# Kernel tuning notes

Measured on AMD Instinct MI355X. Metric: run time of the kernel, lower is better.

The kernel has to match this reference:

```python
import jax, jax.numpy as jnp
import numpy as np

N = 50000   # nodes
E = 800000  # edges
IN, H1, H2, OUT = 256, 512, 1024, 3000
EPS = 1e-5


def _glorot(key, fan_in, fan_out):
    s = jnp.sqrt(6.0 / (fan_in + fan_out)).astype(jnp.float32)
    return jax.random.uniform(key, (fan_in, fan_out), jnp.float32, -s, s)


def setup_inputs() -> dict:
    key = jax.random.key(0)
    ks = jax.random.split(key, 8)
    x = jax.random.normal(ks[0], (N, IN), jnp.float32)
    edge_index = jax.random.randint(ks[1], (2, E), 0, N, jnp.int64)
    edge_attr = jax.random.uniform(ks[2], (E, 3), jnp.float32)
    y = jnp.zeros((N,), jnp.int64)  # single domain -> plain BatchNorm path
    return {
        "x": x, "edge_index": edge_index, "edge_attr": edge_attr, "y": y,
        "W1": _glorot(ks[3], IN, H1), "b1": jnp.zeros((H1,), jnp.float32),
        "g1": jnp.ones((H1,), jnp.float32), "be1": jnp.zeros((H1,), jnp.float32),
        "W2": _glorot(ks[4], H1, H2), "b2": jnp.zeros((H2,), jnp.float32),
        "g2": jnp.ones((H2,), jnp.float32), "be2": jnp.zeros((H2,), jnp.float32),
        "W3": _glorot(ks[5], H2, OUT), "b3": jnp.zeros((OUT,), jnp.float32),
    }


def _gcn_layer(h_in, W, b, src, dst, w):
    # PyG GCNConv: x' = D^{-1/2}(A_w + I)D^{-1/2} x W + b, self-loop weight 1
    h = h_in @ W                                             # [N, F]
    deg = jax.ops.segment_sum(w, dst, num_segments=N) + 1.0  # weighted in-degree + self loop
    dinv = jax.lax.rsqrt(deg)                                # [N]
    coef = dinv[src] * w * dinv[dst]                         # [E]
    agg = jax.ops.segment_sum(coef[:, None] * h[src], dst, num_segments=N)
    return agg + (dinv * dinv)[:, None] * h + b              # self-loop term + bias


def _bn_relu(h, g, b):
    # BatchNorm1d in training mode (batch statistics, biased variance) + ReLU
    m = h.mean(axis=0)
    v = jnp.mean((h - m) ** 2, axis=0)
    return jax.nn.relu((h - m) * jax.lax.rsqrt(v + EPS) * g + b)


def reference(x, edge_index, edge_attr, y, W1, b1, g1, be1, W2, b2, g2, be2, W3, b3):
    src, dst = edge_index[0], edge_index[1]
    w = edge_attr[:, 2]
    h = _bn_relu(_gcn_layer(x, W1, b1, src, dst, w), g1, be1)
    h = _bn_relu(_gcn_layer(h, W2, b2, src, dst, w), g2, be2)
    return _gcn_layer(h, W3, b3, src, dst, w)
```

## Files before the change

kernel.cpp:

```cpp
#include <hip/hip_runtime.h>

#define NN 50000
#define NE 800000
#define EPSV 1e-5f

typedef _Float16 f16;
typedef __attribute__((ext_vector_type(4)))  float f32x4;
typedef __attribute__((ext_vector_type(16))) float f32x16;
typedef __attribute__((ext_vector_type(8)))  f16 f16x8;
typedef __attribute__((ext_vector_type(4)))  f16 f16x4;

static __device__ __forceinline__ int kperm(int k){
  int q = (k>>2)&3;
  int p = ((q&1)<<1) | (q>>1);
  return (k & ~15) + (p<<2) + (k&3);
}

__global__ void k_init_deg(float* __restrict__ deg){
  int i = blockIdx.x*256 + threadIdx.x;
  if (i < NN) deg[i] = 1.0f;
}

__global__ void k_build(const int* __restrict__ ei, const float* __restrict__ ea,
                        int* __restrict__ cnt, float* __restrict__ deg){
  int e = blockIdx.x*256 + threadIdx.x;
  if (e < NE){
    int d = ei[NE + e];
    atomicAdd(&cnt[d], 1);
    atomicAdd(&deg[d], ea[3*e+2]);
  }
}

__global__ void k_fin_deg(const float* __restrict__ deg, float* __restrict__ dinv,
                          float* __restrict__ dinv2){
  int i = blockIdx.x*256 + threadIdx.x;
  if (i < NN){ float r = rsqrtf(deg[i]); dinv[i] = r; dinv2[i] = r*r; }
}

__global__ __launch_bounds__(1024) void k_scan(const int* __restrict__ cnt,
                                               int* __restrict__ rowptr,
                                               int* __restrict__ cursor){
  __shared__ int sums[1024];
  int t = threadIdx.x;
  int b0 = t*49, b1 = b0+49; if (b0 > NN) b0 = NN; if (b1 > NN) b1 = NN;
  int s = 0;
  for (int i = b0; i < b1; ++i) s += cnt[i];
  sums[t] = s; __syncthreads();
  for (int o = 1; o < 1024; o <<= 1){
    int v = (t >= o) ? sums[t-o] : 0;
    __syncthreads();
    sums[t] += v;
    __syncthreads();
  }
  int p = sums[t] - s;
  for (int i = b0; i < b1; ++i){ rowptr[i] = p; cursor[i] = p; p += cnt[i]; }
  if (t == 1023) rowptr[NN] = sums[1023];
}

__global__ void k_fill(const int* __restrict__ ei, const float* __restrict__ ea,
                       const float* __restrict__ dinv, int* __restrict__ cursor,
                       int* __restrict__ csrc, float* __restrict__ ccf){
  int e = blockIdx.x*256 + threadIdx.x;
  if (e < NE){
    int s = ei[e], d = ei[NE+e];
    float w = ea[3*e+2];
    int p = atomicAdd(&cursor[d], 1);
    csrc[p] = s;
    ccf[p] = dinv[s]*w*dinv[d];
  }
}

__global__ void k_xconv(const float* __restrict__ x, f16* __restrict__ xh){
  int idx = blockIdx.x*256 + threadIdx.x;
  if (idx >= NN*64) return;
  int node = idx >> 6, k = (idx & 63)*4;
  f32x4 v = *(const f32x4*)(x + (size_t)node*256 + k);
  f16x4 h;
  #pragma unroll
  for (int j=0;j<4;++j) h[j] = (f16)v[j];
  *(f16x4*)(xh + (size_t)node*256 + kperm(k)) = h;
}

__global__ void k_w16(const float* __restrict__ W, f16* __restrict__ Wt,
                      int K, int M, int Mpad){
  int idx = blockIdx.x*256 + threadIdx.x;
  if (idx >= K*Mpad) return;
  int k = idx / Mpad, n = idx % Mpad;
  float v = (n < M) ? W[(size_t)k*M + n] : 0.f;
  Wt[(size_t)n*K + kperm(k)] = (f16)v;
}

template<int K, bool BN>
__global__ __launch_bounds__(256) void k_agg16(
    const f16* __restrict__ H, const int* __restrict__ rp,
    const int* __restrict__ cs, const float* __restrict__ cf,
    const float* __restrict__ dinv2,
    const float* __restrict__ s1, const float* __restrict__ s2,
    const float* __restrict__ g, const float* __restrict__ be,
    f16* __restrict__ outp)
{
  const int tid = threadIdx.x;
  int node, c;
  if (K == 256){
    node = blockIdx.x*8 + (tid>>5);
    c = (tid&31)*8;
  } else {
    node = blockIdx.x*4 + (tid>>6);
    c = (blockIdx.y<<9) + (tid&63)*8;
  }
  if (node >= NN) return;
  float av[8], bv[8];
  if (BN){
    int qa0 = kperm(c), qa1 = kperm(c+4);
    #pragma unroll
    for (int j=0;j<8;++j){
      int ac = (j<4) ? qa0+j : qa1+(j-4);
      float mm = s1[c+j]*(1.f/NN);
      float var = s2[c+j]*(1.f/NN) - mm*mm;
      float sc = rsqrtf(var+EPSV)*g[ac];
      av[j] = sc;
      bv[j] = fmaf(-mm, sc, be[ac]);
    }
  }
  f16x8 hv = *(const f16x8*)(H + (size_t)node*K + c);
  float d2 = dinv2[node];
  float acc[8];
  #pragma unroll
  for (int j=0;j<8;++j){
    float v = (float)hv[j];
    if (BN){ v = fmaf(v, av[j], bv[j]); v = v > 0.f ? v : 0.f; }
    acc[j] = d2*v;
  }
  int e0 = rp[node], e1 = rp[node+1];
  for (int e = e0; e < e1; ++e){
    int s = cs[e]; float w = cf[e];
    f16x8 v8 = *(const f16x8*)(H + (size_t)s*K + c);
    #pragma unroll
    for (int j=0;j<8;++j){
      float v = (float)v8[j];
      if (BN){ v = fmaf(v, av[j], bv[j]); v = v > 0.f ? v : 0.f; }
      acc[j] += w*v;
    }
  }
  f16x8 o;
  #pragma unroll
  for (int j=0;j<8;++j) o[j] = (f16)acc[j];
  *(f16x8*)(outp + (size_t)node*K + c) = o;
}

template<bool STATS>
__global__ __launch_bounds__(256) void k_gemm16(
    const f16* __restrict__ A, const f16* __restrict__ B,
    const float* __restrict__ bias, float* __restrict__ Cf,
    f16* __restrict__ Ch, float* __restrict__ s1, float* __restrict__ s2,
    int K, int M)
{
  __shared__ f16 Ah[2][4096];
  __shared__ f16 Bh[2][4096];
  const int tid  = threadIdx.x;
  const int lane = tid & 63;
  const int wave = tid >> 6;
  const int wr = wave >> 1, wc = wave & 1;

  int nwg = gridDim.x*gridDim.y;
  int bid = blockIdx.y*gridDim.x + blockIdx.x;
  if ((nwg & 7) == 0){
    int cpx = nwg >> 3;
    bid = (bid & 7)*cpx + (bid >> 3);
  }
  const int bx = bid % gridDim.x, by = bid / gridDim.x;
  const int row0 = by*128, col0 = bx*128;

  f32x16 acc[2][2];
  #pragma unroll
  for (int m=0;m<2;++m)
    #pragma unroll
    for (int n=0;n<2;++n)
      #pragma unroll
      for (int t=0;t<16;++t) acc[m][n][t] = 0.f;

  auto stage = [&](int buf, int k0){
    #pragma unroll
    for (int i=0;i<2;++i){
      int phys = i*256 + tid;
      int rr = phys >> 2, cp = phys & 3;
      int sc2 = cp ^ ((rr>>1)&3);
      const f16* srcA = A + (size_t)(row0+rr)*K + k0 + sc2*8;
      const f16* srcB = B + (size_t)(col0+rr)*K + k0 + sc2*8;
      f16* dstA = &Ah[buf][(size_t)(i*256 + (wave<<6))*8];
      f16* dstB = &Bh[buf][(size_t)(i*256 + (wave<<6))*8];
      __builtin_amdgcn_global_load_lds((const unsigned int*)srcA, (unsigned int*)dstA, 16, 0, 0);
      __builtin_amdgcn_global_load_lds((const unsigned int*)srcB, (unsigned int*)dstB, 16, 0, 0);
    }
  };

  stage(0, 0);
  __syncthreads();
  const int nT = K >> 5;
  for (int t = 0; t < nT; ++t){
    const int cur = t & 1;
    if (t + 1 < nT) stage(cur^1, (t+1) << 5);

    const int hg = lane >> 5;
    #pragma unroll
    for (int c2=0;c2<2;++c2){
      f16x8 fa[2], fb[2];
      #pragma unroll
      for (int m=0;m<2;++m){
        int r = wr*64 + m*32 + (lane&31);
        int u = c2*2 + hg;
        fa[m] = *(const f16x8*)&Ah[cur][r*32 + ((u ^ ((r>>1)&3))<<3)];
      }
      #pragma unroll
      for (int n=0;n<2;++n){
        int r = wc*64 + n*32 + (lane&31);
        int u = c2*2 + hg;
        fb[n] = *(const f16x8*)&Bh[cur][r*32 + ((u ^ ((r>>1)&3))<<3)];
      }
      #pragma unroll
      for (int m=0;m<2;++m)
        #pragma unroll
        for (int n=0;n<2;++n)
          acc[m][n] = __builtin_amdgcn_mfma_f32_32x32x16_f16(fa[m], fb[n], acc[m][n], 0,0,0);
    }
    __syncthreads();
  }

  #pragma unroll
  for (int n=0;n<2;++n){
    int cg = col0 + wc*64 + n*32 + (lane&31);
    if (STATS){
      int cp = kperm(cg);
      float sum = 0.f, sq = 0.f;
      #pragma unroll
      for (int m=0;m<2;++m){
        #pragma unroll
        for (int t=0;t<16;++t){
          int rg = row0 + wr*64 + m*32 + (t&3) + ((t>>2)&3)*8 + ((lane>>5)<<2);
          if (rg < NN){
            float v = acc[m][n][t];
            sum += v; sq += v*v;
            Ch[(size_t)rg*M + cp] = (f16)v;
          }
        }
      }
      atomicAdd(&s1[cp], sum);
      atomicAdd(&s2[cp], sq);
    } else {
      float bv = (cg < M) ? bias[cg] : 0.f;
      #pragma unroll
      for (int m=0;m<2;++m){
        #pragma unroll
        for (int t=0;t<16;++t){
          int rg = row0 + wr*64 + m*32 + (t&3) + ((t>>2)&3)*8 + ((lane>>5)<<2);
          if (rg < NN && cg < M)
            __builtin_nontemporal_store(acc[m][n][t] + bv, &Cf[(size_t)rg*M + cg]);
        }
      }
    }
  }
}

extern "C" void kernel_launch(void* const* d_in, const int* in_sizes, int n_in,
                              void* d_out, int out_size, void* d_ws, size_t ws_size,
                              hipStream_t stream){
  const float* x   = (const float*)d_in[0];
  const int*   ei  = (const int*)d_in[1];
  const float* ea  = (const float*)d_in[2];
  const float* W1  = (const float*)d_in[4];
  const float* g1  = (const float*)d_in[6];
  const float* be1 = (const float*)d_in[7];
  const float* W2  = (const float*)d_in[8];
  const float* g2  = (const float*)d_in[10];
  const float* be2 = (const float*)d_in[11];
  const float* W3  = (const float*)d_in[12];
  const float* b3  = (const float*)d_in[13];
  float* out = (float*)d_out;

  char* p = (char*)d_ws;
  int*   cnt    = (int*)p;   p += (size_t)NN*4;
  int*   cursor = (int*)p;   p += (size_t)NN*4;
  int*   rowptr = (int*)p;   p += (size_t)(NN+4)*4;
  float* deg    = (float*)p; p += (size_t)NN*4;
  float* dinv   = (float*)p; p += (size_t)NN*4;
  float* dinv2  = (float*)p; p += (size_t)NN*4;
  int*   csrc   = (int*)p;   p += (size_t)NE*4;
  float* ccf    = (float*)p; p += (size_t)NE*4;
  f16*   Wt     = (f16*)p;   p += (size_t)3072*1024*2;
  float* s1a    = (float*)p; p += 1024*4;
  float* s2a    = (float*)p; p += 1024*4;
  float* s1b    = (float*)p; p += 1024*4;
  float* s2b    = (float*)p; p += 1024*4;
  f16*   aggh   = (f16*)p;   p += (size_t)50176*1024*2;

  f16* xh  = (f16*)out;
  f16* h1h = xh  + (size_t)NN*256;
  f16* h2h = h1h + (size_t)NN*512;

  const int T = 256;
  const int gN = (NN+T-1)/T, gE = NE/T;
  const int GR = (NN+127)/128;

  hipMemsetAsync(cnt, 0, (size_t)NN*4, stream);
  hipMemsetAsync(s1a, 0, 4*1024*4, stream);
  k_init_deg<<<gN,T,0,stream>>>(deg);
  k_build<<<gE,T,0,stream>>>(ei, ea, cnt, deg);
  k_fin_deg<<<gN,T,0,stream>>>(deg, dinv, dinv2);
  k_scan<<<1,1024,0,stream>>>(cnt, rowptr, cursor);
  k_fill<<<gE,T,0,stream>>>(ei, ea, dinv, cursor, csrc, ccf);
  k_xconv<<<(NN*64+T-1)/T,T,0,stream>>>(x, xh);

  k_agg16<256,false><<<dim3(NN/8,1),T,0,stream>>>(xh, rowptr, csrc, ccf, dinv2,
                                                  nullptr,nullptr,nullptr,nullptr, aggh);
  k_w16<<<(256*512)/T,T,0,stream>>>(W1, Wt, 256, 512, 512);
  k_gemm16<true><<<dim3(4,GR),T,0,stream>>>(aggh, Wt, nullptr, nullptr, h1h, s1a, s2a, 256, 512);

  k_agg16<512,true><<<dim3(NN/4,1),T,0,stream>>>(h1h, rowptr, csrc, ccf, dinv2,
                                                 s1a, s2a, g1, be1, aggh);
  k_w16<<<(512*1024)/T,T,0,stream>>>(W2, Wt, 512, 1024, 1024);
  k_gemm16<true><<<dim3(8,GR),T,0,stream>>>(aggh, Wt, nullptr, nullptr, h2h, s1b, s2b, 512, 1024);

  k_agg16<1024,true><<<dim3(NN/4,2),T,0,stream>>>(h2h, rowptr, csrc, ccf, dinv2,
                                                  s1b, s2b, g2, be2, aggh);
  k_w16<<<(1024*3072)/T,T,0,stream>>>(W3, Wt, 1024, 3000, 3072);
  k_gemm16<false><<<dim3(24,GR),T,0,stream>>>(aggh, Wt, b3, out, nullptr, nullptr, nullptr, 1024, 3000);
}
```

Baseline: 1.700 ms.

## Enlarge GEMM tiles to 256x256 with K-step 64 and a new LDS swizzle

Replaces the 128x128 GEMM tile with a 256x256 output tile per 256-thread block, using a 4x4 array of 32x32 MFMA accumulators per wave and a K step of 64. Each thread now stages whole 128-byte row chunks through global_load_lds with an XOR-based swizzle on the column chunk. The goal is to double operand reuse per LDS byte and cut global/L2 traffic and the number of blocks for the three dense GEMMs. In exchange it uses 128 KB of LDS and far more accumulator registers, so only one block fits per CU. It also pads rows to 50176, which relies on the aggregation buffer's padding and on the Wt buffer having a 3072-column layout.

```diff
diff --git a/kernel.cpp b/kernel.cpp
--- a/kernel.cpp
+++ b/kernel.cpp
@@ -149,18 +149,20 @@
 }
 
 template<bool STATS>
-__global__ __launch_bounds__(256) void k_gemm16(
+__global__ __launch_bounds__(256,1) void k_gemm256(
     const f16* __restrict__ A, const f16* __restrict__ B,
     const float* __restrict__ bias, float* __restrict__ Cf,
     f16* __restrict__ Ch, float* __restrict__ s1, float* __restrict__ s2,
     int K, int M)
 {
-  __shared__ f16 Ah[2][4096];
-  __shared__ f16 Bh[2][4096];
+  __shared__ f16 Ah[2][16384];
+  __shared__ f16 Bh[2][16384];
   const int tid  = threadIdx.x;
   const int lane = tid & 63;
   const int wave = tid >> 6;
   const int wr = wave >> 1, wc = wave & 1;
+  const int hg = lane >> 5;
+  const int rl = lane & 31;
 
   int nwg = gridDim.x*gridDim.y;
   int bid = blockIdx.y*gridDim.x + blockIdx.x;
@@ -169,74 +171,74 @@
     bid = (bid & 7)*cpx + (bid >> 3);
   }
   const int bx = bid % gridDim.x, by = bid / gridDim.x;
-  const int row0 = by*128, col0 = bx*128;
-
-  f32x16 acc[2][2];
-  #pragma unroll
-  for (int m=0;m<2;++m)
-    #pragma unroll
-    for (int n=0;n<2;++n)
+  const int row0 = by*256, col0 = bx*256;
+
+  f32x16 acc[4][4];
+  #pragma unroll
+  for (int m=0;m<4;++m)
+    #pragma unroll
+    for (int n=0;n<4;++n)
       #pragma unroll
       for (int t=0;t<16;++t) acc[m][n][t] = 0.f;
 
+  const f16* rowA = A + (size_t)(row0 + tid)*K;
+  const f16* rowB = B + (size_t)(col0 + tid)*K;
+  const int xo = tid & 7;
+
   auto stage = [&](int buf, int k0){
     #pragma unroll
-    for (int i=0;i<2;++i){
-      int phys = i*256 + tid;
-      int rr = phys >> 2, cp = phys & 3;
-      int sc2 = cp ^ ((rr>>1)&3);
-      const f16* srcA = A + (size_t)(row0+rr)*K + k0 + sc2*8;
-      const f16* srcB = B + (size_t)(col0+rr)*K + k0 + sc2*8;
-      f16* dstA = &Ah[buf][(size_t)(i*256 + (wave<<6))*8];
-      f16* dstB = &Bh[buf][(size_t)(i*256 + (wave<<6))*8];
-      __builtin_amdgcn_global_load_lds((const unsigned int*)srcA, (unsigned int*)dstA, 16, 0, 0);
-      __builtin_amdgcn_global_load_lds((const unsigned int*)srcB, (unsigned int*)dstB, 16, 0, 0);
+    for (int i=0;i<8;++i){
+      int cA = i ^ xo;
+      f16* dstA = &Ah[buf][i*2048 + wave*512];
+      __builtin_amdgcn_global_load_lds((const unsigned int*)(rowA + k0 + cA*8),
+                                       (unsigned int*)dstA, 16, 0, 0);
+      f16* dstB = &Bh[buf][i*2048 + wave*512];
+      __builtin_amdgcn_global_load_lds((const unsigned int*)(rowB + k0 + cA*8),
+                                       (unsigned int*)dstB, 16, 0, 0);
     }
   };
 
   stage(0, 0);
   __syncthreads();
-  const int nT = K >> 5;
+  const int nT = K >> 6;
   for (int t = 0; t < nT; ++t){
     const int cur = t & 1;
-    if (t + 1 < nT) stage(cur^1, (t+1) << 5);
-
-    const int hg = lane >> 5;
-    #pragma unroll
-    for (int c2=0;c2<2;++c2){
-      f16x8 fa[2], fb[2];
-      #pragma unroll
-      for (int m=0;m<2;++m){
-        int r = wr*64 + m*32 + (lane&31);
-        int u = c2*2 + hg;
-        fa[m] = *(const f16x8*)&Ah[cur][r*32 + ((u ^ ((r>>1)&3))<<3)];
+    if (t + 1 < nT) stage(cur^1, (t+1) << 6);
+
+    #pragma unroll
+    for (int g=0; g<4; ++g){
+      const int u = g*2 + hg;
+      f16x8 fa[4], fb[4];
+      #pragma unroll
+      for (int m=0;m<4;++m){
+        int r = wr*128 + m*32 + rl;
+        fa[m] = *(const f16x8*)&Ah[cur][((u ^ (r&7))<<11) + (r<<3)];
       }
       #pragma unroll
-      for (int n=0;n<2;++n){
-        int r = wc*64 + n*32 + (lane&31);
-        int u = c2*2 + hg;
-        fb[n] = *(const f16x8*)&Bh[cur][r*32 + ((u ^ ((r>>1)&3))<<3)];
+      for (int n=0;n<4;++n){
+        int r = wc*128 + n*32 + rl;
+        fb[n] = *(const f16x8*)&Bh[cur][((u ^ (r&7))<<11) + (r<<3)];
       }
       #pragma unroll
-      for (int m=0;m<2;++m)
+      for (int m=0;m<4;++m)
         #pragma unroll
-        for (int n=0;n<2;++n)
+        for (int n=0;n<4;++n)
           acc[m][n] = __builtin_amdgcn_mfma_f32_32x32x16_f16(fa[m], fb[n], acc[m][n], 0,0,0);
     }
     __syncthreads();
   }
 
   #pragma unroll
-  for (int n=0;n<2;++n){
-    int cg = col0 + wc*64 + n*32 + (lane&31);
+  for (int n=0;n<4;++n){
+    int cg = col0 + wc*128 + n*32 + rl;
     if (STATS){
       int cp = kperm(cg);
       float sum = 0.f, sq = 0.f;
       #pragma unroll
-      for (int m=0;m<2;++m){
+      for (int m=0;m<4;++m){
         #pragma unroll
         for (int t=0;t<16;++t){
-          int rg = row0 + wr*64 + m*32 + (t&3) + ((t>>2)&3)*8 + ((lane>>5)<<2);
+          int rg = row0 + wr*128 + m*32 + (t&3) + ((t>>2)&3)*8 + (hg<<2);
           if (rg < NN){
             float v = acc[m][n][t];
             sum += v; sq += v*v;
@@ -249,10 +251,10 @@
     } else {
       float bv = (cg < M) ? bias[cg] : 0.f;
       #pragma unroll
-      for (int m=0;m<2;++m){
+      for (int m=0;m<4;++m){
         #pragma unroll
         for (int t=0;t<16;++t){
-          int rg = row0 + wr*64 + m*32 + (t&3) + ((t>>2)&3)*8 + ((lane>>5)<<2);
+          int rg = row0 + wr*128 + m*32 + (t&3) + ((t>>2)&3)*8 + (hg<<2);
           if (rg < NN && cg < M)
             __builtin_nontemporal_store(acc[m][n][t] + bv, &Cf[(size_t)rg*M + cg]);
         }
@@ -299,7 +301,6 @@
 
   const int T = 256;
   const int gN = (NN+T-1)/T, gE = NE/T;
-  const int GR = (NN+127)/128;
 
   hipMemsetAsync(cnt, 0, (size_t)NN*4, stream);
   hipMemsetAsync(s1a, 0, 4*1024*4, stream);
@@ -313,15 +314,15 @@
   k_agg16<256,false><<<dim3(NN/8,1),T,0,stream>>>(xh, rowptr, csrc, ccf, dinv2,
                                                   nullptr,nullptr,nullptr,nullptr, aggh);
   k_w16<<<(256*512)/T,T,0,stream>>>(W1, Wt, 256, 512, 512);
-  k_gemm16<true><<<dim3(4,GR),T,0,stream>>>(aggh, Wt, nullptr, nullptr, h1h, s1a, s2a, 256, 512);
+  k_gemm256<true><<<dim3(2,196),T,0,stream>>>(aggh, Wt, nullptr, nullptr, h1h, s1a, s2a, 256, 512);
 
   k_agg16<512,true><<<dim3(NN/4,1),T,0,stream>>>(h1h, rowptr, csrc, ccf, dinv2,
                                                  s1a, s2a, g1, be1, aggh);
   k_w16<<<(512*1024)/T,T,0,stream>>>(W2, Wt, 512, 1024, 1024);
-  k_gemm16<true><<<dim3(8,GR),T,0,stream>>>(aggh, Wt, nullptr, nullptr, h2h, s1b, s2b, 512, 1024);
+  k_gemm256<true><<<dim3(4,196),T,0,stream>>>(aggh, Wt, nullptr, nullptr, h2h, s1b, s2b, 512, 1024);
 
   k_agg16<1024,true><<<dim3(NN/4,2),T,0,stream>>>(h2h, rowptr, csrc, ccf, dinv2,
                                                   s1b, s2b, g2, be2, aggh);
   k_w16<<<(1024*3072)/T,T,0,stream>>>(W3, Wt, 1024, 3000, 3072);
-  k_gemm16<false><<<dim3(24,GR),T,0,stream>>>(aggh, Wt, b3, out, nullptr, nullptr, nullptr, 1024, 3000);
-}
+  k_gemm256<false><<<dim3(12,196),T,0,stream>>>(aggh, Wt, b3, out, nullptr, nullptr, nullptr, 1024, 3000);
+}
```

Measured after the change: 2.324 ms. 36.7% more time.
